# Performance work log

Hardware: AMD Instinct MI355X
Metric: run time of the kernel (lower is better)

## Reference

```python
import jax, jax.numpy as jnp
from jax import lax
import numpy as np

FRAME = 160  # frame_size


def setup_inputs() -> dict:
    key = jax.random.key(0)
    ks = jax.random.split(key, 24)
    rn = lambda k, s, sc=0.08: jax.random.normal(k, s, jnp.float32) * sc
    bs, F, cs = 16, 19, (19 - 4) * FRAME  # cs = 2400
    inp = {
        "pcm": jax.random.randint(ks[0], (bs, cs, 3), 0, 256),
        "feat": jax.random.normal(ks[1], (bs, F, 38), jnp.float32),
        "pitch": jax.random.randint(ks[2], (bs, F, 1), 0, 256),
        "emb_pcm": rn(ks[3], (256, 128), 0.5),
        "emb_pitch": rn(ks[4], (256, 64), 0.05),
        "conv1_w": rn(ks[5], (128, 102, 3)),
        "conv1_b": jnp.zeros((128,), jnp.float32),
        "conv2_w": rn(ks[6], (128, 128, 3)),
        "conv2_b": jnp.zeros((128,), jnp.float32),
        "d1_w": rn(ks[7], (128, 128)),
        "d1_b": jnp.zeros((128,), jnp.float32),
        "d2_w": rn(ks[8], (128, 128)),
        "d2_b": jnp.zeros((128,), jnp.float32),
        "g1_wih": rn(ks[9], (1152, 512)),
        "g1_whh": rn(ks[10], (1152, 384)),
        "g1_bih": jnp.zeros((1152,), jnp.float32),
        "g1_bhh": jnp.zeros((1152,), jnp.float32),
        "g2_wih": rn(ks[11], (48, 512)),
        "g2_whh": rn(ks[12], (48, 16)),
        "g2_bih": jnp.zeros((48,), jnp.float32),
        "g2_bhh": jnp.zeros((48,), jnp.float32),
        "fc1_w": rn(ks[13], (256, 16), 0.25),
        "fc1_b": jnp.zeros((256,), jnp.float32),
        "fc2_w": rn(ks[14], (256, 16), 0.25),
        "fc2_b": jnp.zeros((256,), jnp.float32),
        "gamma1": jnp.ones((256,), jnp.float32),
        "gamma2": jnp.ones((256,), jnp.float32),
    }
    return inp


def _gru(x, h0, wih, whh, bih, bhh):
    # x: [B,T,D]; h0: [B,H]; torch GRU gate order (r, z, n)
    gx = jnp.einsum('btd,gd->btg', x, wih) + bih  # [B,T,3H]

    def step(h, gx_t):
        gh = h @ whh.T + bhh
        xr, xz, xn = jnp.split(gx_t, 3, axis=-1)
        hr, hz, hn = jnp.split(gh, 3, axis=-1)
        r = jax.nn.sigmoid(xr + hr)
        z = jax.nn.sigmoid(xz + hz)
        n = jnp.tanh(xn + r * hn)
        h = (1.0 - z) * n + z * h
        return h, h

    h_last, out = lax.scan(step, h0, jnp.swapaxes(gx, 0, 1))
    return jnp.swapaxes(out, 0, 1), h_last


def _conv1d(x, w, b):
    # x: [B,C,L], w: [O,I,K]; VALID padding (prepad mode)
    y = lax.conv_general_dilated(x, w, (1,), 'VALID',
                                 dimension_numbers=('NCH', 'OIH', 'NCH'))
    return y + b[None, :, None]


def reference(pcm, feat, pitch, emb_pcm, emb_pitch, conv1_w, conv1_b,
              conv2_w, conv2_b, d1_w, d1_b, d2_w, d2_b,
              g1_wih, g1_whh, g1_bih, g1_bhh,
              g2_wih, g2_whh, g2_bih, g2_bhh,
              fc1_w, fc1_b, fc2_w, fc2_b, gamma1, gamma2):
    bs, cs = pcm.shape[0], pcm.shape[1]
    # ---- encode ----
    p = emb_pitch[pitch[..., 0]]                       # [B,F,64]
    f = jnp.concatenate([feat, p], axis=2)             # [B,F,102]
    f = jnp.transpose(f, (0, 2, 1))                    # NCW
    f = jnp.tanh(_conv1d(f, conv1_w, conv1_b))
    f = jnp.tanh(_conv1d(f, conv2_w, conv2_b))
    f = jnp.transpose(f, (0, 2, 1))                    # [B,F-4,128]
    f = jnp.tanh(jnp.tanh(f @ d1_w.T + d1_b) @ d2_w.T + d2_b)
    # ---- decode ----
    e = emb_pcm[pcm].reshape(bs, cs, -1)               # [B,cs,384]
    rfeat = jnp.repeat(f, FRAME, axis=1)               # [B,cs,128]
    rnn_in = jnp.concatenate([e, rfeat], axis=-1)      # [B,cs,512]
    h1 = jnp.zeros((bs, g1_whh.shape[1]), jnp.float32)
    out, _ = _gru(rnn_in, h1, g1_wih, g1_whh, g1_bih, g1_bhh)
    rnn_in = jnp.concatenate([out, rfeat], axis=-1)    # [B,cs,512]
    h2 = jnp.zeros((bs, g2_whh.shape[1]), jnp.float32)
    out, _ = _gru(rnn_in, h2, g2_wih, g2_whh, g2_bih, g2_bhh)  # [B,cs,16]
    # ---- MDense head ----
    y1 = jnp.tanh(out @ fc1_w.T + fc1_b)
    y2 = jnp.tanh(out @ fc2_w.T + fc2_b)
    prob = gamma1 * y1 + gamma2 * y2                   # [B,cs,256]
    return prob
```

## Files before the change

### kernel.cpp

```cpp
#include <hip/hip_runtime.h>
#include <hip/hip_bf16.h>
#include <math.h>

typedef __attribute__((ext_vector_type(4))) float f32x4;
typedef __attribute__((ext_vector_type(8))) short bf16x8;

#define NB1 24

__device__ __forceinline__ unsigned short f2bf(float f){
  union { float f; unsigned int i; } c; c.f = f;
  return (unsigned short)((c.i + 0x7fffu + ((c.i >> 16) & 1u)) >> 16);
}
__device__ __forceinline__ float sigm(float x){
  return 1.0f / (1.0f + exp2f(-1.4426950408889634f * x));
}
__device__ __forceinline__ float tanh_(float x){
  float e = exp2f(2.8853900817779268f * x);
  return 1.0f - 2.0f / (e + 1.0f);
}

__global__ void __launch_bounds__(128) encoder_kernel(
    const float* __restrict__ feat, const int* __restrict__ pitch,
    const float* __restrict__ emb_pitch,
    const float* __restrict__ w1, const float* __restrict__ b1,
    const float* __restrict__ w2, const float* __restrict__ b2,
    const float* __restrict__ d1w, const float* __restrict__ d1b,
    const float* __restrict__ d2w, const float* __restrict__ d2b,
    float* __restrict__ fout)
{
  int b = blockIdx.x, tid = threadIdx.x;
  __shared__ float xin[19][104];
  __shared__ float t1[17][128];
  __shared__ float t2[15][128];
  __shared__ float t3[15][128];
  for (int idx = tid; idx < 19*38; idx += 128){ int l = idx/38, c = idx-l*38; xin[l][c] = feat[(b*19+l)*38+c]; }
  for (int idx = tid; idx < 19*64; idx += 128){ int l = idx/64, c = idx-l*64; xin[l][38+c] = emb_pitch[pitch[b*19+l]*64+c]; }
  __syncthreads();
  {
    int c = tid;
    float acc[17];
    float bias = b1[c];
#pragma unroll
    for (int l=0;l<17;++l) acc[l]=bias;
    for (int i=0;i<102;++i){
      const float* wp = w1 + (c*102+i)*3;
      float w0 = wp[0], wk1 = wp[1], wk2 = wp[2];
      float x[19];
#pragma unroll
      for (int l=0;l<19;++l) x[l]=xin[l][i];
#pragma unroll
      for (int l=0;l<17;++l) acc[l] += w0*x[l] + wk1*x[l+1] + wk2*x[l+2];
    }
#pragma unroll
    for (int l=0;l<17;++l) t1[l][c] = tanh_(acc[l]);
  }
  __syncthreads();
  {
    int c = tid;
    float acc[15];
    float bias = b2[c];
#pragma unroll
    for (int l=0;l<15;++l) acc[l]=bias;
    for (int i=0;i<128;++i){
      const float* wp = w2 + (c*128+i)*3;
      float w0 = wp[0], wk1 = wp[1], wk2 = wp[2];
      float x[17];
#pragma unroll
      for (int l=0;l<17;++l) x[l]=t1[l][i];
#pragma unroll
      for (int l=0;l<15;++l) acc[l] += w0*x[l] + wk1*x[l+1] + wk2*x[l+2];
    }
#pragma unroll
    for (int l=0;l<15;++l) t2[l][c] = tanh_(acc[l]);
  }
  __syncthreads();
  {
    int c = tid;
    float acc[15];
    float bias = d1b[c];
#pragma unroll
    for (int l=0;l<15;++l) acc[l]=bias;
    for (int i=0;i<128;++i){
      float w = d1w[c*128+i];
#pragma unroll
      for (int l=0;l<15;++l) acc[l] += w*t2[l][i];
    }
#pragma unroll
    for (int l=0;l<15;++l) t3[l][c] = tanh_(acc[l]);
  }
  __syncthreads();
  {
    int c = tid;
    float acc[15];
    float bias = d2b[c];
#pragma unroll
    for (int l=0;l<15;++l) acc[l]=bias;
    for (int i=0;i<128;++i){
      float w = d2w[c*128+i];
#pragma unroll
      for (int l=0;l<15;++l) acc[l] += w*t3[l][i];
    }
#pragma unroll
    for (int l=0;l<15;++l) fout[(b*15+l)*128+c] = tanh_(acc[l]);
  }
}

__global__ void __launch_bounds__(256) tables_kernel(
    const float* __restrict__ emb_pcm, const float* __restrict__ wih1,
    float* __restrict__ Tp)
{
  int v = blockIdx.x & 255, j = blockIdx.x >> 8;
  int tid = threadIdx.x;
  __shared__ float e[128];
  if (tid < 128) e[tid] = emb_pcm[v*128+tid];
  __syncthreads();
  for (int g = tid; g < 1152; g += 256){
    const float* wrow = wih1 + g*512 + j*128;
    float acc = 0.f;
    for (int i=0;i<128;i+=4){
      float4 u = *(const float4*)(wrow + i);
      acc += u.x*e[i+0]+u.y*e[i+1]+u.z*e[i+2]+u.w*e[i+3];
    }
    int gate = g/384, jg = g - gate*384;
    Tp[(j*256+v)*1536 + jg*4 + gate] = acc;
  }
}

__global__ void __launch_bounds__(256) fg_kernel(
    const float* __restrict__ f,
    const float* __restrict__ wih1, const float* __restrict__ bih1,
    const float* __restrict__ wih2, const float* __restrict__ bih2,
    float* __restrict__ Fg1p, float* __restrict__ Fg2)
{
  int bf_ = blockIdx.x;
  int tid = threadIdx.x;
  __shared__ float fr[128];
  if (tid < 128) fr[tid] = f[bf_*128+tid];
  __syncthreads();
  for (int g = tid; g < 1152; g += 256){
    const float* wrow = wih1 + g*512 + 384;
    float acc = bih1[g];
    for (int i=0;i<128;i+=4){
      float4 u = *(const float4*)(wrow + i);
      acc += u.x*fr[i+0]+u.y*fr[i+1]+u.z*fr[i+2]+u.w*fr[i+3];
    }
    int gate = g/384, jg = g - gate*384;
    Fg1p[bf_*1536 + jg*4 + gate] = acc;
  }
  if (tid < 48){
    const float* wrow = wih2 + tid*512 + 384;
    float acc = bih2[tid];
    for (int i=0;i<128;i+=4){
      float4 u = *(const float4*)(wrow + i);
      acc += u.x*fr[i+0]+u.y*fr[i+1]+u.z*fr[i+2]+u.w*fr[i+3];
    }
    Fg2[bf_*48+tid] = acc;
  }
}

__global__ void __launch_bounds__(64) gru1_scan(
    const int* __restrict__ pcm, const float* __restrict__ whh,
    const float* __restrict__ bhh,
    const float* __restrict__ Tp, const float* __restrict__ Fg1p,
    unsigned short* __restrict__ hbuf, int* __restrict__ flags,
    unsigned short* __restrict__ out1)
{
  int blk = blockIdx.x;
  int l = threadIdx.x;
  int q = l >> 4, n = l & 15;
  int jg = blk*16 + n;
  int jg4 = jg*4;

  bf16x8 W[3][12];
#pragma unroll
  for (int gate=0; gate<3; ++gate){
    const float* wr = whh + (gate*384 + jg)*384;
#pragma unroll
    for (int kk=0; kk<12; ++kk){
#pragma unroll
      for (int jj=0; jj<8; ++jj) W[gate][kk][jj] = (short)f2bf(wr[kk*32 + q*8 + jj]);
    }
  }
  float bhr = bhh[jg], bhz = bhh[384+jg], bhn = bhh[768+jg];
  float hown[4] = {0.f,0.f,0.f,0.f};
  const float* T1p = Tp + 256*1536;
  const float* T2p = Tp + 2*256*1536;
  int frame = 0, cnt = 0;

  for (int t = 1; t <= 2400; ++t){
    int tt = t-1;
    float xr[4], xz[4], xn[4];
#pragma unroll
    for (int r=0;r<4;++r){
      int b = (q<<2) + r;
      const int* pp = pcm + (b*2400 + tt)*3;
      int i0 = pp[0], i1 = pp[1], i2 = pp[2];
      float4 a0 = *(const float4*)(Tp  + i0*1536 + jg4);
      float4 a1 = *(const float4*)(T1p + i1*1536 + jg4);
      float4 a2 = *(const float4*)(T2p + i2*1536 + jg4);
      float4 af = *(const float4*)(Fg1p + (b*15+frame)*1536 + jg4);
      xr[r] = a0.x+a1.x+a2.x+af.x;
      xz[r] = a0.y+a1.y+a2.y+af.y;
      xn[r] = a0.z+a1.z+a2.z+af.z;
    }
    f32x4 accr = {0.f,0.f,0.f,0.f}, accz = {0.f,0.f,0.f,0.f}, accn = {0.f,0.f,0.f,0.f};
    if (t > 1){
      int need = t-1;
      for (;;){
        int v = need;
        if (l < NB1) v = __hip_atomic_load(flags + l*16, __ATOMIC_RELAXED, __HIP_MEMORY_SCOPE_AGENT);
        if (__all(v >= need)) break;
      }
      __threadfence();
      const unsigned short* hrow = hbuf + (tt&1)*6144 + n*384 + q*8;
      bf16x8 A[12];
#pragma unroll
      for (int kk=0;kk<12;++kk) A[kk] = *(const bf16x8*)(hrow + kk*32);
#pragma unroll
      for (int kk=0;kk<12;++kk){
        accr = __builtin_amdgcn_mfma_f32_16x16x32_bf16(A[kk], W[0][kk], accr, 0,0,0);
        accz = __builtin_amdgcn_mfma_f32_16x16x32_bf16(A[kk], W[1][kk], accz, 0,0,0);
        accn = __builtin_amdgcn_mfma_f32_16x16x32_bf16(A[kk], W[2][kk], accn, 0,0,0);
      }
    }
    unsigned short hb[4];
#pragma unroll
    for (int r=0;r<4;++r){
      float hr = accr[r]+bhr, hz = accz[r]+bhz, hn_ = accn[r]+bhn;
      float rg = sigm(xr[r]+hr);
      float zg = sigm(xz[r]+hz);
      float ng = tanh_(xn[r]+rg*hn_);
      float h = (1.f-zg)*ng + zg*hown[r];
      hown[r] = h;
      hb[r] = f2bf(h);
      hbuf[(t&1)*6144 + ((q<<2)+r)*384 + jg] = hb[r];
    }
    __threadfence();
    if (l == 0) __hip_atomic_store(flags + blk*16, t, __ATOMIC_RELEASE, __HIP_MEMORY_SCOPE_AGENT);
#pragma unroll
    for (int r=0;r<4;++r) out1[(((q<<2)+r)*2400 + tt)*384 + jg] = hb[r];
    if (++cnt == 160){ cnt = 0; ++frame; }
  }
}

__global__ void __launch_bounds__(256) gx2_kernel(
    const unsigned short* __restrict__ out1, const float* __restrict__ wih2,
    const float* __restrict__ Fg2, float* __restrict__ gx2)
{
  int tile = blockIdx.x, b = blockIdx.y;
  int tid = threadIdx.x;
  __shared__ float wl[48*388];
  __shared__ unsigned short xl[16*392];
  for (int v = tid; v < 48*96; v += 256){
    int row = v/96, c4 = (v - row*96)*4;
    *(float4*)(wl + row*388 + c4) = *(const float4*)(wih2 + row*512 + c4);
  }
  for (int v = tid; v < 16*48; v += 256){
    int row = v/48, c8 = (v - row*48)*8;
    *(uint4*)(xl + row*392 + c8) = *(const uint4*)(out1 + (b*2400 + tile*16 + row)*384 + c8);
  }
  __syncthreads();
  for (int o = tid; o < 768; o += 256){
    int g = o >> 4, tl = o & 15;
    int tg = tile*16 + tl, fr = tg/160;
    float acc = Fg2[(b*15+fr)*48 + g];
    const unsigned short* xp = xl + tl*392;
    const float* wp = wl + g*388;
    for (int i=0;i<384;++i){
      union { unsigned int u; float f; } cv; cv.u = ((unsigned int)xp[i]) << 16;
      acc += cv.f * wp[i];
    }
    gx2[(b*2400+tg)*48 + g] = acc;
  }
}

__global__ void __launch_bounds__(64) gru2_scan(
    const float* __restrict__ gx2, const float* __restrict__ whh2,
    const float* __restrict__ bhh2, float* __restrict__ out2)
{
  int b = blockIdx.x, l = threadIdx.x;
  int q = l >> 4, n = l & 15;
  __shared__ unsigned short hs[32];
  __shared__ float gxs[16*48];
  if (l < 32) hs[l] = 0;
  bf16x8 Wr = {0,0,0,0,0,0,0,0}, Wz = {0,0,0,0,0,0,0,0}, Wn = {0,0,0,0,0,0,0,0};
  if (q < 2){
#pragma unroll
    for (int jj=0; jj<8; ++jj){
      Wr[jj] = (short)f2bf(whh2[(n)*16 + q*8 + jj]);
      Wz[jj] = (short)f2bf(whh2[(16+n)*16 + q*8 + jj]);
      Wn[jj] = (short)f2bf(whh2[(32+n)*16 + q*8 + jj]);
    }
  }
  float bh_r=0.f, bh_z=0.f, bh_n=0.f, h=0.f;
  if (l < 16){ bh_r = bhh2[l]; bh_z = bhh2[16+l]; bh_n = bhh2[32+l]; }
  const float* src = gx2 + b*2400*48;
  float4 p0 = ((const float4*)src)[l];
  float4 p1 = ((const float4*)src)[l+64];
  float4 p2 = ((const float4*)src)[l+128];
  __syncthreads();
  for (int t=0; t<2400; ++t){
    int ph = t & 15;
    if (ph == 0){
      __syncthreads();
      ((float4*)gxs)[l] = p0; ((float4*)gxs)[l+64] = p1; ((float4*)gxs)[l+128] = p2;
      if (t+16 < 2400){
        const float4* s2 = (const float4*)(src + (t+16)*48);
        p0 = s2[l]; p1 = s2[l+64]; p2 = s2[l+128];
      }
      __syncthreads();
    }
    bf16x8 a = {0,0,0,0,0,0,0,0};
    if (n == 0) a = *(const bf16x8*)(hs + q*8);
    f32x4 z4 = {0.f,0.f,0.f,0.f};
    f32x4 dr = __builtin_amdgcn_mfma_f32_16x16x32_bf16(a, Wr, z4, 0,0,0);
    f32x4 dz = __builtin_amdgcn_mfma_f32_16x16x32_bf16(a, Wz, z4, 0,0,0);
    f32x4 dn = __builtin_amdgcn_mfma_f32_16x16x32_bf16(a, Wn, z4, 0,0,0);
    if (l < 16){
      const float* g = gxs + ph*48;
      float rg = sigm(g[l] + dr[0] + bh_r);
      float zg = sigm(g[16+l] + dz[0] + bh_z);
      float ng = tanh_(g[32+l] + rg*(dn[0] + bh_n));
      h = (1.f - zg)*ng + zg*h;
      hs[l] = f2bf(h);
      out2[(b*2400+t)*16 + l] = h;
    }
    __syncthreads();
  }
}

__global__ void __launch_bounds__(256) head_kernel(
    const float* __restrict__ out2,
    const float* __restrict__ fc1w, const float* __restrict__ fc1b,
    const float* __restrict__ fc2w, const float* __restrict__ fc2b,
    const float* __restrict__ g1, const float* __restrict__ g2,
    float* __restrict__ out)
{
  int blk = blockIdx.x;
  int b = blk/150, tile = blk - b*150;
  int c = threadIdx.x;
  __shared__ float s[256];
  float w1[16], w2[16];
#pragma unroll
  for (int k=0;k<16;k+=4){
    float4 u = *(const float4*)(fc1w + c*16 + k);
    w1[k]=u.x; w1[k+1]=u.y; w1[k+2]=u.z; w1[k+3]=u.w;
    float4 v = *(const float4*)(fc2w + c*16 + k);
    w2[k]=v.x; w2[k+1]=v.y; w2[k+2]=v.z; w2[k+3]=v.w;
  }
  float b1 = fc1b[c], b2 = fc2b[c];
  float ga = g1[c], gb = g2[c];
  int base = b*2400 + tile*16;
  s[c] = out2[base*16 + c];
  __syncthreads();
  for (int tl=0; tl<16; ++tl){
    float a1=b1, a2=b2;
#pragma unroll
    for (int k=0;k<16;++k){ float x = s[tl*16+k]; a1 += x*w1[k]; a2 += x*w2[k]; }
    float y = ga*tanh_(a1) + gb*tanh_(a2);
    out[(base+tl)*256 + c] = y;
  }
}

extern "C" void kernel_launch(void* const* d_in, const int* in_sizes, int n_in,
                              void* d_out, int out_size, void* d_ws, size_t ws_size,
                              hipStream_t stream)
{
  const int*   pcm      = (const int*)d_in[0];
  const float* feat     = (const float*)d_in[1];
  const int*   pitch    = (const int*)d_in[2];
  const float* emb_pcm  = (const float*)d_in[3];
  const float* emb_pit  = (const float*)d_in[4];
  const float* conv1_w  = (const float*)d_in[5];
  const float* conv1_b  = (const float*)d_in[6];
  const float* conv2_w  = (const float*)d_in[7];
  const float* conv2_b  = (const float*)d_in[8];
  const float* d1_w     = (const float*)d_in[9];
  const float* d1_b     = (const float*)d_in[10];
  const float* d2_w     = (const float*)d_in[11];
  const float* d2_b     = (const float*)d_in[12];
  const float* g1_wih   = (const float*)d_in[13];
  const float* g1_whh   = (const float*)d_in[14];
  const float* g1_bih   = (const float*)d_in[15];
  const float* g1_bhh   = (const float*)d_in[16];
  const float* g2_wih   = (const float*)d_in[17];
  const float* g2_whh   = (const float*)d_in[18];
  const float* g2_bih   = (const float*)d_in[19];
  const float* g2_bhh   = (const float*)d_in[20];
  const float* fc1_w    = (const float*)d_in[21];
  const float* fc1_b    = (const float*)d_in[22];
  const float* fc2_w    = (const float*)d_in[23];
  const float* fc2_b    = (const float*)d_in[24];
  const float* gamma1   = (const float*)d_in[25];
  const float* gamma2   = (const float*)d_in[26];

  char* ws = (char*)d_ws;
  int*            flags = (int*)(ws + 0);
  float*          f_ws  = (float*)(ws + 2048);
  float*          Tp    = (float*)(ws + 131072);
  float*          Fg1p  = (float*)(ws + 4849664);
  float*          Fg2   = (float*)(ws + 6324224);
  unsigned short* hbuf  = (unsigned short*)(ws + 6370304);
  unsigned short* out1  = (unsigned short*)(ws + 6394880);
  float*          gx2   = (float*)(ws + 35886080);
  float*          out2  = (float*)(ws + 43258880);

  hipMemsetAsync(flags, 0, 2048, stream);
  encoder_kernel<<<16, 128, 0, stream>>>(feat, pitch, emb_pit, conv1_w, conv1_b,
                                         conv2_w, conv2_b, d1_w, d1_b, d2_w, d2_b, f_ws);
  tables_kernel<<<768, 256, 0, stream>>>(emb_pcm, g1_wih, Tp);
  fg_kernel<<<240, 256, 0, stream>>>(f_ws, g1_wih, g1_bih, g2_wih, g2_bih, Fg1p, Fg2);
  gru1_scan<<<NB1, 64, 0, stream>>>(pcm, g1_whh, g1_bhh, Tp, Fg1p, hbuf, flags, out1);
  gx2_kernel<<<dim3(150,16), 256, 0, stream>>>(out1, g2_wih, Fg2, gx2);
  gru2_scan<<<16, 64, 0, stream>>>(gx2, g2_whh, g2_bhh, out2);
  head_kernel<<<2400, 256, 0, stream>>>(out2, fc1_w, fc1_b, fc2_w, fc2_b, gamma1, gamma2,
                                        (float*)d_out);
}
```

Baseline: 13.47 ms.

## Replace flag-based GRU1 step barrier with tagged hidden-state words

The cross-block handshake in the persistent GRU1 scan changes. Instead of each block publishing a flag after a threadfence and every block polling all flags before reading the hidden state, each 64-bit word now carries two bf16 hidden values plus the timestep tag, written with relaxed atomics. Readers issue their loads early, overlapping them with the input-gate gathers, and re-poll only stale words. This removes the fences, the flag round trip and the memset, at the cost of wider hbuf traffic and a memory-ordering scheme that relies on 64-bit atomic store and load being atomic. The first timestep is also peeled out of the loop.

```diff
diff --git a/kernel.cpp b/kernel.cpp
--- a/kernel.cpp
+++ b/kernel.cpp
@@ -158,11 +158,11 @@
   }
 }
 
-__global__ void __launch_bounds__(64) gru1_scan(
+__global__ void __launch_bounds__(64,1) gru1_scan(
     const int* __restrict__ pcm, const float* __restrict__ whh,
     const float* __restrict__ bhh,
     const float* __restrict__ Tp, const float* __restrict__ Fg1p,
-    unsigned short* __restrict__ hbuf, int* __restrict__ flags,
+    unsigned long long* __restrict__ hbuf,
     unsigned short* __restrict__ out1)
 {
   int blk = blockIdx.x;
@@ -170,6 +170,8 @@
   int q = l >> 4, n = l & 15;
   int jg = blk*16 + n;
   int jg4 = jg*4;
+  bool evenlane = ((n & 1) == 0);
+  int wstore = blk*8 + (n >> 1);
 
   bf16x8 W[3][12];
 #pragma unroll
@@ -187,8 +189,60 @@
   const float* T2p = Tp + 2*256*1536;
   int frame = 0, cnt = 0;
 
-  for (int t = 1; t <= 2400; ++t){
+  {
+    float xr[4], xz[4], xn[4];
+#pragma unroll
+    for (int r=0;r<4;++r){
+      int b = (q<<2) + r;
+      const int* pp = pcm + (b*2400 + 0)*3;
+      int i0 = pp[0], i1 = pp[1], i2 = pp[2];
+      float4 a0 = *(const float4*)(Tp  + i0*1536 + jg4);
+      float4 a1 = *(const float4*)(T1p + i1*1536 + jg4);
+      float4 a2 = *(const float4*)(T2p + i2*1536 + jg4);
+      float4 af = *(const float4*)(Fg1p + (b*15+0)*1536 + jg4);
+      xr[r] = a0.x+a1.x+a2.x+af.x;
+      xz[r] = a0.y+a1.y+a2.y+af.y;
+      xn[r] = a0.z+a1.z+a2.z+af.z;
+    }
+    float hnew[4];
+    unsigned short hb16[4];
+#pragma unroll
+    for (int r=0;r<4;++r){
+      float rg = sigm(xr[r]+bhr);
+      float zg = sigm(xz[r]+bhz);
+      float ng = tanh_(xn[r]+rg*bhn);
+      float h = (1.f-zg)*ng;
+      hown[r] = h; hnew[r] = h; hb16[r] = f2bf(h);
+    }
+    unsigned long long* dst = hbuf + (1&1)*3072;
+#pragma unroll
+    for (int r=0;r<4;++r){
+      float partner = __shfl_xor(hnew[r], 1);
+      if (evenlane){
+        unsigned int lo = (unsigned int)hb16[r] | ((unsigned int)f2bf(partner) << 16);
+        unsigned long long wv = ((unsigned long long)1u << 32) | lo;
+        __hip_atomic_store(dst + ((q<<2)+r)*192 + wstore, wv, __ATOMIC_RELAXED, __HIP_MEMORY_SCOPE_AGENT);
+      }
+    }
+#pragma unroll
+    for (int r=0;r<4;++r) out1[(((q<<2)+r)*2400 + 0)*384 + jg] = hb16[r];
+    cnt = 1;
+  }
+
+  for (int t = 2; t <= 2400; ++t){
     int tt = t-1;
+    unsigned int tag = (unsigned int)tt;
+    int p = tt & 1;
+    const unsigned long long* hb = hbuf + p*3072 + n*192;
+
+    unsigned long long w[48];
+#pragma unroll
+    for (int kk=0;kk<12;++kk){
+#pragma unroll
+      for (int i=0;i<4;++i)
+        w[kk*4+i] = __hip_atomic_load(hb + kk*16 + q*4 + i, __ATOMIC_RELAXED, __HIP_MEMORY_SCOPE_AGENT);
+    }
+
     float xr[4], xz[4], xn[4];
 #pragma unroll
     for (int r=0;r<4;++r){
@@ -203,27 +257,34 @@
       xz[r] = a0.y+a1.y+a2.y+af.y;
       xn[r] = a0.z+a1.z+a2.z+af.z;
     }
+
+    for (;;){
+      int bad = 0;
+#pragma unroll
+      for (int s=0;s<48;++s){
+        if ((unsigned int)(w[s] >> 32) != tag){
+          w[s] = __hip_atomic_load(hb + (s>>2)*16 + q*4 + (s&3), __ATOMIC_RELAXED, __HIP_MEMORY_SCOPE_AGENT);
+          bad = 1;
+        }
+      }
+      if (!__any(bad)) break;
+    }
+
     f32x4 accr = {0.f,0.f,0.f,0.f}, accz = {0.f,0.f,0.f,0.f}, accn = {0.f,0.f,0.f,0.f};
-    if (t > 1){
-      int need = t-1;
-      for (;;){
-        int v = need;
-        if (l < NB1) v = __hip_atomic_load(flags + l*16, __ATOMIC_RELAXED, __HIP_MEMORY_SCOPE_AGENT);
-        if (__all(v >= need)) break;
-      }
-      __threadfence();
-      const unsigned short* hrow = hbuf + (tt&1)*6144 + n*384 + q*8;
-      bf16x8 A[12];
-#pragma unroll
-      for (int kk=0;kk<12;++kk) A[kk] = *(const bf16x8*)(hrow + kk*32);
-#pragma unroll
-      for (int kk=0;kk<12;++kk){
-        accr = __builtin_amdgcn_mfma_f32_16x16x32_bf16(A[kk], W[0][kk], accr, 0,0,0);
-        accz = __builtin_amdgcn_mfma_f32_16x16x32_bf16(A[kk], W[1][kk], accz, 0,0,0);
-        accn = __builtin_amdgcn_mfma_f32_16x16x32_bf16(A[kk], W[2][kk], accn, 0,0,0);
-      }
-    }
-    unsigned short hb[4];
+#pragma unroll
+    for (int kk=0;kk<12;++kk){
+      union { bf16x8 v; unsigned int u[4]; } a;
+      a.u[0] = (unsigned int)w[kk*4+0];
+      a.u[1] = (unsigned int)w[kk*4+1];
+      a.u[2] = (unsigned int)w[kk*4+2];
+      a.u[3] = (unsigned int)w[kk*4+3];
+      accr = __builtin_amdgcn_mfma_f32_16x16x32_bf16(a.v, W[0][kk], accr, 0,0,0);
+      accz = __builtin_amdgcn_mfma_f32_16x16x32_bf16(a.v, W[1][kk], accz, 0,0,0);
+      accn = __builtin_amdgcn_mfma_f32_16x16x32_bf16(a.v, W[2][kk], accn, 0,0,0);
+    }
+
+    float hnew[4];
+    unsigned short hb16[4];
 #pragma unroll
     for (int r=0;r<4;++r){
       float hr = accr[r]+bhr, hz = accz[r]+bhz, hn_ = accn[r]+bhn;
@@ -231,14 +292,21 @@
       float zg = sigm(xz[r]+hz);
       float ng = tanh_(xn[r]+rg*hn_);
       float h = (1.f-zg)*ng + zg*hown[r];
-      hown[r] = h;
-      hb[r] = f2bf(h);
-      hbuf[(t&1)*6144 + ((q<<2)+r)*384 + jg] = hb[r];
-    }
-    __threadfence();
-    if (l == 0) __hip_atomic_store(flags + blk*16, t, __ATOMIC_RELEASE, __HIP_MEMORY_SCOPE_AGENT);
-#pragma unroll
-    for (int r=0;r<4;++r) out1[(((q<<2)+r)*2400 + tt)*384 + jg] = hb[r];
+      hown[r] = h; hnew[r] = h; hb16[r] = f2bf(h);
+    }
+    unsigned long long* dst = hbuf + (t&1)*3072;
+#pragma unroll
+    for (int r=0;r<4;++r){
+      float partner = __shfl_xor(hnew[r], 1);
+      if (evenlane){
+        unsigned int lo = (unsigned int)hb16[r] | ((unsigned int)f2bf(partner) << 16);
+        unsigned long long wv = ((unsigned long long)(unsigned int)t << 32) | lo;
+        __hip_atomic_store(dst + ((q<<2)+r)*192 + wstore, wv, __ATOMIC_RELAXED, __HIP_MEMORY_SCOPE_AGENT);
+      }
+    }
+#pragma unroll
+    for (int r=0;r<4;++r) out1[(((q<<2)+r)*2400 + tt)*384 + jg] = hb16[r];
+
     if (++cnt == 160){ cnt = 0; ++frame; }
   }
 }
@@ -395,22 +463,20 @@
   const float* gamma2   = (const float*)d_in[26];
 
   char* ws = (char*)d_ws;
-  int*            flags = (int*)(ws + 0);
-  float*          f_ws  = (float*)(ws + 2048);
-  float*          Tp    = (float*)(ws + 131072);
-  float*          Fg1p  = (float*)(ws + 4849664);
-  float*          Fg2   = (float*)(ws + 6324224);
-  unsigned short* hbuf  = (unsigned short*)(ws + 6370304);
-  unsigned short* out1  = (unsigned short*)(ws + 6394880);
-  float*          gx2   = (float*)(ws + 35886080);
-  float*          out2  = (float*)(ws + 43258880);
-
-  hipMemsetAsync(flags, 0, 2048, stream);
+  float*              f_ws  = (float*)(ws + 0);
+  float*              Tp    = (float*)(ws + 131072);
+  float*              Fg1p  = (float*)(ws + 4849664);
+  float*              Fg2   = (float*)(ws + 6324224);
+  unsigned long long* hbuf  = (unsigned long long*)(ws + 6370304);
+  unsigned short*     out1  = (unsigned short*)(ws + 6419456);
+  float*              gx2   = (float*)(ws + 35910656);
+  float*              out2  = (float*)(ws + 43283456);
+
   encoder_kernel<<<16, 128, 0, stream>>>(feat, pitch, emb_pit, conv1_w, conv1_b,
                                          conv2_w, conv2_b, d1_w, d1_b, d2_w, d2_b, f_ws);
   tables_kernel<<<768, 256, 0, stream>>>(emb_pcm, g1_wih, Tp);
   fg_kernel<<<240, 256, 0, stream>>>(f_ws, g1_wih, g1_bih, g2_wih, g2_bih, Fg1p, Fg2);
-  gru1_scan<<<NB1, 64, 0, stream>>>(pcm, g1_whh, g1_bhh, Tp, Fg1p, hbuf, flags, out1);
+  gru1_scan<<<NB1, 64, 0, stream>>>(pcm, g1_whh, g1_bhh, Tp, Fg1p, hbuf, out1);
   gx2_kernel<<<dim3(150,16), 256, 0, stream>>>(out1, g2_wih, Fg2, gx2);
   gru2_scan<<<16, 64, 0, stream>>>(gx2, g2_whh, g2_bhh, out2);
   head_kernel<<<2400, 256, 0, stream>>>(out2, fc1_w, fc1_b, fc2_w, fc2_b, gamma1, gamma2,
```

Result: faster. 12.83 ms (-4.7%).
